# Optimization experiments

Hardware: AMD Instinct MI355X
Metric: run time of the kernel (lower is better)

The kernel has to match this reference:

```python
import jax, jax.numpy as jnp
import numpy as np

B, C, H, W = 16, 64, 1024, 16  # requires C*W == H per the module's implicit view/matmul constraint
C8 = C // 8


def setup_inputs() -> dict:
    key = jax.random.key(0)
    ks = jax.random.split(key, 7)
    s_in = 1.0 / np.sqrt(C)
    return {
        "x": jax.random.normal(ks[0], (B, C, H, W), dtype=jnp.float32),
        "Wq": jax.random.normal(ks[1], (C8, C), dtype=jnp.float32) * s_in,
        "bq": jax.random.normal(ks[2], (C8,), dtype=jnp.float32) * 0.01,
        "Wk": jax.random.normal(ks[3], (C8, C), dtype=jnp.float32) * s_in,
        "bk": jax.random.normal(ks[4], (C8,), dtype=jnp.float32) * 0.01,
        "Wv": jax.random.normal(ks[5], (C, C), dtype=jnp.float32) * s_in,
        "bv": jax.random.normal(ks[6], (C,), dtype=jnp.float32) * 0.01,
    }


def conv1x1(x, w, b):
    # 1x1 conv == per-pixel channel mixing: [B,C,H,W] x [O,C] -> [B,O,H,W]
    return jnp.einsum("bchw,oc->bohw", x, w) + b[None, :, None, None]


def reference(x, Wq, bq, Wk, bk, Wv, bv):
    b, c, h, w = x.shape
    q = conv1x1(x, Wq, bq)  # [B, C/8, H, W]
    k = conv1x1(x, Wk, bk)  # [B, C/8, H, W]
    v = conv1x1(x, Wv, bv)  # [B, C, H, W]
    # Faithful to torch .view(B, -1, H): row-major reshape, NOT a transpose.
    qf = jnp.swapaxes(q.reshape(b, -1, h), 1, 2)  # [B, H, C8*W]
    kf = k.reshape(b, -1, h)                      # [B, C8*W, H]
    vf = v.reshape(b, -1, h)                      # [B, C*W, H] (C*W == H)
    scores = jax.nn.softmax(jnp.matmul(qf, kf), axis=-1)  # [B, H, H]
    attended = jnp.matmul(scores, vf)             # [B, H, H]
    attended = attended.reshape(v.shape)          # [B, C, H, W]
    return x + attended
```

## Files before the change

### kernel.cpp

```cpp
#include <hip/hip_runtime.h>
#include <stdint.h>

typedef uint32_t u32;
typedef __attribute__((ext_vector_type(4))) float f32x4;
typedef __attribute__((ext_vector_type(8))) short short8;

#define NBATCH 16
#define NPIX   16384
#define NPB    1048576

__device__ __forceinline__ ushort f2bf(float f) {
  u32 b = __builtin_bit_cast(u32, f);
  return (ushort)((b + 0x7FFFu + ((b >> 16) & 1u)) >> 16);
}
__device__ __forceinline__ float bf2f(ushort h) {
  return __builtin_bit_cast(float, (u32)h << 16);
}

__device__ __forceinline__ void gload16(const void* g, void* l) {
  __builtin_amdgcn_global_load_lds(
      (const __attribute__((address_space(1))) u32*)g,
      (__attribute__((address_space(3))) u32*)l,
      16, 0, 0);
}

__global__ void prep_w2(const float* __restrict__ Wq, const float* __restrict__ bq,
                        const float* __restrict__ Wk, const float* __restrict__ bk,
                        const float* __restrict__ Wv, const float* __restrict__ bv,
                        ushort* __restrict__ Wpk, float* __restrict__ bpk)
{
  int gid = blockIdx.x * 256 + threadIdx.x;
  if (gid < 12288) {
    int m = gid >> 7, kk = gid & 127;
    int ch = kk & 63;
    ushort outv = 0;
    if (m < 8) {
      float wv = Wq[m * 64 + ch];
      ushort h = f2bf(wv);
      outv = (kk < 64) ? h : f2bf(wv - bf2f(h));
    } else if (m < 16) {
      float wv = Wk[(m - 8) * 64 + ch];
      ushort h = f2bf(wv);
      outv = (kk < 64) ? h : f2bf(wv - bf2f(h));
    } else if (m < 80) {
      outv = (kk < 64) ? f2bf(Wv[(m - 16) * 64 + ch]) : (ushort)0;
    }
    Wpk[gid] = outv;
  } else if (gid < 12368) {
    int o = gid - 12288;
    bpk[o] = (o < 8) ? bq[o] : (o < 16 ? bk[o - 8] : bv[o - 16]);
  }
}

__global__ __launch_bounds__(256) void proj12(
    const float* __restrict__ x, const ushort* __restrict__ Wpk,
    const float* __restrict__ bpk,
    ushort* __restrict__ Qt2, ushort* __restrict__ Kt2,
    ushort* __restrict__ Vt)
{
  __shared__ __align__(16) char smem[65536];
  int t = threadIdx.x;
  int w = t >> 6, lane = t & 63;
  int l15 = lane & 15, l4 = lane >> 4;

  int g = blockIdx.x;
  int lin = (g & 7) * 128 + (g >> 3);
  int b = lin >> 6;
  int l0 = (lin & 63) << 4;

  const uint4* Wp4 = (const uint4*)Wpk;
  uint4 Afrag[12];
  #pragma unroll
  for (int kc = 0; kc < 4; ++kc)
    Afrag[kc] = Wp4[l15 * 16 + kc * 4 + l4];
  #pragma unroll
  for (int mt = 1; mt < 5; ++mt)
    #pragma unroll
    for (int kc = 0; kc < 2; ++kc)
      Afrag[2 + mt * 2 + kc] = Wp4[(mt * 16 + l15) * 16 + kc * 4 + l4];
  __builtin_amdgcn_sched_barrier(0);

  #pragma unroll
  for (int c = 0; c < 2; ++c) {
    const float* xb = x + (size_t)b * NPB + l0 + c * 8;
    float* xs = (float*)(smem + c * 32768);
    #pragma unroll
    for (int it = 0; it < 8; ++it) {
      int f0 = (it * 4 + w) * 64;
      int f = f0 + lane;
      int ch = f >> 5, r2 = f & 31, tc = r2 >> 1, half = r2 & 1;
      gload16(xb + (size_t)ch * NPIX + tc * 1024 + half * 4, xs + f0 * 4);
    }
  }
  asm volatile("s_waitcnt vmcnt(8)" ::: "memory");
  __builtin_amdgcn_sched_barrier(0);
  __builtin_amdgcn_s_barrier();

  auto do_chunk = [&](char* region, int lc) {
    float* xs = (float*)region;
    f32x4 acc[5][2];
    #pragma unroll
    for (int mt = 0; mt < 5; ++mt) {
      f32x4 bv4;
      #pragma unroll
      for (int r = 0; r < 4; ++r) bv4[r] = bpk[mt * 16 + l4 * 4 + r];
      acc[mt][0] = bv4; acc[mt][1] = bv4;
    }
    #pragma unroll
    for (int i = 0; i < 2; ++i) {
      int px = (w * 2 + i) * 16 + l15;
      u32 xr[16];
      #pragma unroll
      for (int kc = 0; kc < 2; ++kc)
        #pragma unroll
        for (int j = 0; j < 8; ++j)
          xr[kc * 8 + j] = ((const u32*)xs)[(kc * 32 + l4 * 8 + j) * 128 + px];
      uint4 bxh[2], bxl[2];
      #pragma unroll
      for (int kc = 0; kc < 2; ++kc)
        #pragma unroll
        for (int p = 0; p < 4; ++p) {
          u32 a = xr[kc * 8 + 2 * p], cc = xr[kc * 8 + 2 * p + 1];
          ((u32*)&bxh[kc])[p] = (a >> 16) | (cc & 0xFFFF0000u);
          float fa = __builtin_bit_cast(float, a) -
                     __builtin_bit_cast(float, a & 0xFFFF0000u);
          float fc = __builtin_bit_cast(float, cc) -
                     __builtin_bit_cast(float, cc & 0xFFFF0000u);
          u32 la = __builtin_bit_cast(u32, fa), lc2 = __builtin_bit_cast(u32, fc);
          ((u32*)&bxl[kc])[p] = (la >> 16) | (lc2 & 0xFFFF0000u);
        }
      short8 h0 = __builtin_bit_cast(short8, bxh[0]);
      short8 h1 = __builtin_bit_cast(short8, bxh[1]);
      short8 s0 = __builtin_bit_cast(short8, bxl[0]);
      short8 s1 = __builtin_bit_cast(short8, bxl[1]);
      acc[0][i] = __builtin_amdgcn_mfma_f32_16x16x32_bf16(
          __builtin_bit_cast(short8, Afrag[0]), h0, acc[0][i], 0, 0, 0);
      acc[0][i] = __builtin_amdgcn_mfma_f32_16x16x32_bf16(
          __builtin_bit_cast(short8, Afrag[1]), h1, acc[0][i], 0, 0, 0);
      acc[0][i] = __builtin_amdgcn_mfma_f32_16x16x32_bf16(
          __builtin_bit_cast(short8, Afrag[0]), s0, acc[0][i], 0, 0, 0);
      acc[0][i] = __builtin_amdgcn_mfma_f32_16x16x32_bf16(
          __builtin_bit_cast(short8, Afrag[1]), s1, acc[0][i], 0, 0, 0);
      acc[0][i] = __builtin_amdgcn_mfma_f32_16x16x32_bf16(
          __builtin_bit_cast(short8, Afrag[2]), h0, acc[0][i], 0, 0, 0);
      acc[0][i] = __builtin_amdgcn_mfma_f32_16x16x32_bf16(
          __builtin_bit_cast(short8, Afrag[3]), h1, acc[0][i], 0, 0, 0);
      #pragma unroll
      for (int mt = 1; mt < 5; ++mt) {
        acc[mt][i] = __builtin_amdgcn_mfma_f32_16x16x32_bf16(
            __builtin_bit_cast(short8, Afrag[2 + mt * 2]), h0, acc[mt][i], 0, 0, 0);
        acc[mt][i] = __builtin_amdgcn_mfma_f32_16x16x32_bf16(
            __builtin_bit_cast(short8, Afrag[3 + mt * 2]), h1, acc[mt][i], 0, 0, 0);
      }
    }
    __syncthreads();

    float*  qkl = (float*)region;
    ushort* vl  = (ushort*)(region + 16 * 132 * 4);
    #pragma unroll
    for (int i = 0; i < 2; ++i) {
      int px = (w * 2 + i) * 16 + l15;
      #pragma unroll
      for (int r = 0; r < 4; ++r)
        qkl[(l4 * 4 + r) * 132 + px] = acc[0][i][r];
      #pragma unroll
      for (int mt = 1; mt < 5; ++mt)
        #pragma unroll
        for (int r = 0; r < 4; ++r)
          vl[((mt - 1) * 16 + l4 * 4 + r) * 136 + px] = f2bf(acc[mt][i][r]);
    }
    __syncthreads();

    if (t < 128) {
      int l = t >> 4, tcc = t & 15;
      size_t lrow = (size_t)b * 1024 + lc + l;
      int px = tcc * 8 + l;

      union { ushort s[8]; uint4 v; } qh, ql, kh, kl;
      #pragma unroll
      for (int o = 0; o < 8; ++o) {
        float qv = qkl[o * 132 + px];
        ushort h = f2bf(qv);
        qh.s[o] = h; ql.s[o] = f2bf(qv - bf2f(h));
        float kv = qkl[(8 + o) * 132 + px];
        h = f2bf(kv);
        kh.s[o] = h; kl.s[o] = f2bf(kv - bf2f(h));
      }
      ushort* qrow = Qt2 + lrow * 256 + tcc * 8;
      *(uint4*)qrow         = qh.v;
      *(uint4*)(qrow + 128) = ql.v;
      ushort* krow = Kt2 + lrow * 256 + tcc * 8;
      *(uint4*)krow         = kh.v;
      *(uint4*)(krow + 128) = kl.v;
    } else {
      int t2 = t - 128;
      int l = t2 >> 4, tcc = t2 & 15;
      size_t lrow = (size_t)b * 1024 + lc + l;

      ushort* vrow = Vt + lrow * 1024;
      #pragma unroll
      for (int it = 0; it < 4; ++it) {
        int c2 = (it << 4) + tcc;
        union { ushort s[16]; uint4 q[2]; } ov;
        #pragma unroll
        for (int tt = 0; tt < 16; ++tt)
          ov.s[tt] = vl[c2 * 136 + tt * 8 + l];
        *(uint4*)(vrow + c2 * 16)     = ov.q[0];
        *(uint4*)(vrow + c2 * 16 + 8) = ov.q[1];
      }
    }
  };

  do_chunk(smem, l0);
  do_chunk(smem + 32768, l0 + 8);
}

__global__ __launch_bounds__(512, 4) void gemm_qk2(
    const ushort* __restrict__ A,
    const ushort* __restrict__ B,
    float* __restrict__ C)
{
  __shared__ ushort Asm[8192];
  __shared__ ushort Bsm[16384];
  int t = threadIdx.x;

  int g = blockIdx.x;
  int lin = (g & 7) * 64 + (g >> 3);
  int bz = lin >> 5;
  int r5 = lin & 31;
  int by = r5 >> 2;
  int bx = r5 & 3;
  int m0 = by << 7, n0 = bx << 8;

  const ushort* Ab = A + (size_t)bz * 1024 * 256;
  const ushort* Bb = B + (size_t)bz * 1024 * 256;
  int w = t >> 6, lane = t & 63;
  int wm = w >> 2, wn = w & 3;
  int l15 = lane & 15, l4 = lane >> 4;

  int swc = (t & 7) ^ ((t >> 3) & 7);
  const ushort* pa = Ab + (size_t)(m0 + (t >> 3)) * 256 + swc * 8;
  const ushort* pb = Bb + (size_t)(n0 + (t >> 3)) * 256 + swc * 8;
  int wb = w * 512;

  constexpr int KA[6] = {0, 64, 128, 192, 0, 64};
  constexpr int KB[6] = {0, 64, 0, 64, 128, 192};

  f32x4 acc[4][4] = {};

  for (int it = 0; it < 6; ++it) {
    #pragma unroll
    for (int i = 0; i < 2; ++i)
      gload16(pa + (size_t)i * 64 * 256 + KA[it], Asm + i * 4096 + wb);
    #pragma unroll
    for (int i = 0; i < 4; ++i)
      gload16(pb + (size_t)i * 64 * 256 + KB[it], Bsm + i * 4096 + wb);
    __syncthreads();

    #pragma unroll
    for (int kk = 0; kk < 2; ++kk) {
      short8 af[4], bfr[4];
      #pragma unroll
      for (int mi = 0; mi < 4; ++mi) {
        int rr = (wm << 6) + (mi << 4) + l15;
        af[mi] = __builtin_bit_cast(short8,
            ((const uint4*)Asm)[rr * 8 + ((kk * 4 + l4) ^ (rr & 7))]);
      }
      #pragma unroll
      for (int ni = 0; ni < 4; ++ni) {
        int rr = (wn << 6) + (ni << 4) + l15;
        bfr[ni] = __builtin_bit_cast(short8,
            ((const uint4*)Bsm)[rr * 8 + ((kk * 4 + l4) ^ (rr & 7))]);
      }
      #pragma unroll
      for (int mi = 0; mi < 4; ++mi)
        #pragma unroll
        for (int ni = 0; ni < 4; ++ni)
          acc[mi][ni] = __builtin_amdgcn_mfma_f32_16x16x32_bf16(
              af[mi], bfr[ni], acc[mi][ni], 0, 0, 0);
    }
    __syncthreads();
  }

  #pragma unroll
  for (int mi = 0; mi < 4; ++mi) {
    int rbase = m0 + (wm << 6) + (mi << 4) + (l4 << 2);
    #pragma unroll
    for (int ni = 0; ni < 4; ++ni) {
      int col = n0 + (wn << 6) + (ni << 4) + l15;
      f32x4 v = acc[mi][ni];
      #pragma unroll
      for (int rr = 0; rr < 4; ++rr) {
        size_t idx = ((size_t)bz * 1024 + rbase + rr) * 1024 + col;
        C[idx] = v[rr];
      }
    }
  }
}

__global__ __launch_bounds__(512, 4) void gemm_pv(
    const ushort* __restrict__ A, int lda,
    const ushort* __restrict__ B, int ldb,
    float* __restrict__ C, const float* __restrict__ X)
{
  __shared__ ushort Asm[8192];
  __shared__ ushort Bsm[16384];
  int t = threadIdx.x;

  int g = blockIdx.x;
  int lin = (g & 7) * 64 + (g >> 3);
  int bz = lin >> 5;
  int r5 = lin & 31;
  int by = r5 >> 2;
  int bx = r5 & 3;
  int m0 = by << 7, n0 = bx << 8;

  const ushort* Ab = A + (size_t)bz * 1024 * lda;
  const ushort* Bb = B + (size_t)bz * 1024 * ldb;
  int w = t >> 6, lane = t & 63;
  int wm = w >> 2, wn = w & 3;
  int l15 = lane & 15, l4 = lane >> 4;

  int swc = (t & 7) ^ ((t >> 3) & 7);
  const ushort* pa = Ab + (size_t)(m0 + (t >> 3)) * lda + swc * 8;
  const ushort* pb = Bb + (size_t)(n0 + (t >> 3)) * ldb + swc * 8;
  int wb = w * 512;

  f32x4 acc[4][4] = {};

  for (int it = 0; it < 16; ++it) {
    int k0 = it * 64;
    #pragma unroll
    for (int i = 0; i < 2; ++i)
      gload16(pa + (size_t)i * 64 * lda + k0, Asm + i * 4096 + wb);
    #pragma unroll
    for (int i = 0; i < 4; ++i)
      gload16(pb + (size_t)i * 64 * ldb + k0, Bsm + i * 4096 + wb);
    __syncthreads();

    #pragma unroll
    for (int kk = 0; kk < 2; ++kk) {
      short8 af[4], bfr[4];
      #pragma unroll
      for (int mi = 0; mi < 4; ++mi) {
        int rr = (wm << 6) + (mi << 4) + l15;
        af[mi] = __builtin_bit_cast(short8,
            ((const uint4*)Asm)[rr * 8 + ((kk * 4 + l4) ^ (rr & 7))]);
      }
      #pragma unroll
      for (int ni = 0; ni < 4; ++ni) {
        int rr = (wn << 6) + (ni << 4) + l15;
        bfr[ni] = __builtin_bit_cast(short8,
            ((const uint4*)Bsm)[rr * 8 + ((kk * 4 + l4) ^ (rr & 7))]);
      }
      #pragma unroll
      for (int mi = 0; mi < 4; ++mi)
        #pragma unroll
        for (int ni = 0; ni < 4; ++ni)
          acc[mi][ni] = __builtin_amdgcn_mfma_f32_16x16x32_bf16(
              af[mi], bfr[ni], acc[mi][ni], 0, 0, 0);
    }
    __syncthreads();
  }

  #pragma unroll
  for (int mi = 0; mi < 4; ++mi) {
    int rbase = m0 + (wm << 6) + (mi << 4) + (l4 << 2);
    #pragma unroll
    for (int ni = 0; ni < 4; ++ni) {
      int col = n0 + (wn << 6) + (ni << 4) + l15;
      f32x4 v = acc[mi][ni];
      #pragma unroll
      for (int rr = 0; rr < 4; ++rr) {
        size_t idx = ((size_t)bz * 1024 + rbase + rr) * 1024 + col;
        C[idx] = v[rr] + X[idx];
      }
    }
  }
}

__global__ __launch_bounds__(256) void softmax_rows(float* __restrict__ S)
{
  size_t rowi = blockIdx.x;
  float* srow = S + rowi * 1024;
  int t = threadIdx.x;
  float4 v = ((const float4*)srow)[t];
  float m = fmaxf(fmaxf(v.x, v.y), fmaxf(v.z, v.w));
  #pragma unroll
  for (int off = 32; off > 0; off >>= 1) m = fmaxf(m, __shfl_xor(m, off));
  __shared__ float red[8];
  int wid = t >> 6, lane = t & 63;
  if (lane == 0) red[wid] = m;
  __syncthreads();
  m = fmaxf(fmaxf(red[0], red[1]), fmaxf(red[2], red[3]));
  float e0 = __expf(v.x - m), e1 = __expf(v.y - m);
  float e2 = __expf(v.z - m), e3 = __expf(v.w - m);
  float s = e0 + e1 + e2 + e3;
  #pragma unroll
  for (int off = 32; off > 0; off >>= 1) s += __shfl_xor(s, off);
  if (lane == 0) red[4 + wid] = s;
  __syncthreads();
  s = red[4] + red[5] + red[6] + red[7];
  float inv = 1.0f / s;
  union { ushort h[4]; uint2 q; } pk;
  pk.h[0] = f2bf(e0 * inv); pk.h[1] = f2bf(e1 * inv);
  pk.h[2] = f2bf(e2 * inv); pk.h[3] = f2bf(e3 * inv);
  ((uint2*)srow)[t] = pk.q;
}

extern "C" void kernel_launch(void* const* d_in, const int* in_sizes, int n_in,
                              void* d_out, int out_size, void* d_ws, size_t ws_size,
                              hipStream_t stream) {
  const float* x  = (const float*)d_in[0];
  const float* Wq = (const float*)d_in[1];
  const float* bq = (const float*)d_in[2];
  const float* Wk = (const float*)d_in[3];
  const float* bk = (const float*)d_in[4];
  const float* Wv = (const float*)d_in[5];
  const float* bv = (const float*)d_in[6];
  float* out = (float*)d_out;

  char* wsb = (char*)d_ws;
  ushort* Qt2 = (ushort*)wsb;
  ushort* Kt2 = (ushort*)(wsb + 8388608);
  ushort* Vt  = (ushort*)(wsb + 16777216);
  float*  S   = (float*)(wsb + 50331648);
  ushort* Wpk = (ushort*)(wsb + 117440512);
  float*  bpk = (float*)(wsb + 117440512 + 24576);

  prep_w2<<<49, 256, 0, stream>>>(Wq, bq, Wk, bk, Wv, bv, Wpk, bpk);
  proj12<<<1024, 256, 0, stream>>>(x, Wpk, bpk, Qt2, Kt2, Vt);
  gemm_qk2<<<512, 512, 0, stream>>>(Qt2, Kt2, S);
  softmax_rows<<<16384, 256, 0, stream>>>(S);
  gemm_pv<<<512, 512, 0, stream>>>((const ushort*)S, 2048, Vt, 1024, out, x);
}
```

Baseline: 125.1 us.

## Shrink GEMM tiles to 128x128 with 256 threads and widen projection to 512 threads

The QK and PV GEMMs move from 128x256 tiles with 512 threads (8 waves) to 128x128 tiles with 256 threads (4 waves). This doubles the grid to 1024 blocks, halves the B shared-memory buffer, and raises the occupancy hint to 5 blocks per CU. The projection kernel goes to 512 threads, so each wave handles one pixel group instead of two and issues half as many global-to-LDS loads. The aim is more parallelism and better load balance across CUs, at the cost of less data reuse per tile and extra redundant A/B loads. The wait count and loop trip counts are adjusted to match.

New measurement: 230.4 us. 1.84x slower.

```diff
diff --git a/kernel.cpp b/kernel.cpp
--- a/kernel.cpp
+++ b/kernel.cpp
@@ -52,7 +52,7 @@
   }
 }
 
-__global__ __launch_bounds__(256) void proj12(
+__global__ __launch_bounds__(512) void proj13(
     const float* __restrict__ x, const ushort* __restrict__ Wpk,
     const float* __restrict__ bpk,
     ushort* __restrict__ Qt2, ushort* __restrict__ Kt2,
@@ -85,30 +85,29 @@
     const float* xb = x + (size_t)b * NPB + l0 + c * 8;
     float* xs = (float*)(smem + c * 32768);
     #pragma unroll
-    for (int it = 0; it < 8; ++it) {
-      int f0 = (it * 4 + w) * 64;
+    for (int it = 0; it < 4; ++it) {
+      int f0 = (it * 8 + w) * 64;
       int f = f0 + lane;
       int ch = f >> 5, r2 = f & 31, tc = r2 >> 1, half = r2 & 1;
       gload16(xb + (size_t)ch * NPIX + tc * 1024 + half * 4, xs + f0 * 4);
     }
   }
-  asm volatile("s_waitcnt vmcnt(8)" ::: "memory");
+  asm volatile("s_waitcnt vmcnt(4)" ::: "memory");
   __builtin_amdgcn_sched_barrier(0);
   __builtin_amdgcn_s_barrier();
 
   auto do_chunk = [&](char* region, int lc) {
     float* xs = (float*)region;
-    f32x4 acc[5][2];
+    f32x4 acc[5];
     #pragma unroll
     for (int mt = 0; mt < 5; ++mt) {
       f32x4 bv4;
       #pragma unroll
       for (int r = 0; r < 4; ++r) bv4[r] = bpk[mt * 16 + l4 * 4 + r];
-      acc[mt][0] = bv4; acc[mt][1] = bv4;
-    }
-    #pragma unroll
-    for (int i = 0; i < 2; ++i) {
-      int px = (w * 2 + i) * 16 + l15;
+      acc[mt] = bv4;
+    }
+    {
+      int px = w * 16 + l15;
       u32 xr[16];
       #pragma unroll
       for (int kc = 0; kc < 2; ++kc)
@@ -133,41 +132,40 @@
       short8 h1 = __builtin_bit_cast(short8, bxh[1]);
       short8 s0 = __builtin_bit_cast(short8, bxl[0]);
       short8 s1 = __builtin_bit_cast(short8, bxl[1]);
-      acc[0][i] = __builtin_amdgcn_mfma_f32_16x16x32_bf16(
-          __builtin_bit_cast(short8, Afrag[0]), h0, acc[0][i], 0, 0, 0);
-      acc[0][i] = __builtin_amdgcn_mfma_f32_16x16x32_bf16(
-          __builtin_bit_cast(short8, Afrag[1]), h1, acc[0][i], 0, 0, 0);
-      acc[0][i] = __builtin_amdgcn_mfma_f32_16x16x32_bf16(
-          __builtin_bit_cast(short8, Afrag[0]), s0, acc[0][i], 0, 0, 0);
-      acc[0][i] = __builtin_amdgcn_mfma_f32_16x16x32_bf16(
-          __builtin_bit_cast(short8, Afrag[1]), s1, acc[0][i], 0, 0, 0);
-      acc[0][i] = __builtin_amdgcn_mfma_f32_16x16x32_bf16(
-          __builtin_bit_cast(short8, Afrag[2]), h0, acc[0][i], 0, 0, 0);
-      acc[0][i] = __builtin_amdgcn_mfma_f32_16x16x32_bf16(
-          __builtin_bit_cast(short8, Afrag[3]), h1, acc[0][i], 0, 0, 0);
+      acc[0] = __builtin_amdgcn_mfma_f32_16x16x32_bf16(
+          __builtin_bit_cast(short8, Afrag[0]), h0, acc[0], 0, 0, 0);
+      acc[0] = __builtin_amdgcn_mfma_f32_16x16x32_bf16(
+          __builtin_bit_cast(short8, Afrag[1]), h1, acc[0], 0, 0, 0);
+      acc[0] = __builtin_amdgcn_mfma_f32_16x16x32_bf16(
+          __builtin_bit_cast(short8, Afrag[0]), s0, acc[0], 0, 0, 0);
+      acc[0] = __builtin_amdgcn_mfma_f32_16x16x32_bf16(
+          __builtin_bit_cast(short8, Afrag[1]), s1, acc[0], 0, 0, 0);
+      acc[0] = __builtin_amdgcn_mfma_f32_16x16x32_bf16(
+          __builtin_bit_cast(short8, Afrag[2]), h0, acc[0], 0, 0, 0);
+      acc[0] = __builtin_amdgcn_mfma_f32_16x16x32_bf16(
+          __builtin_bit_cast(short8, Afrag[3]), h1, acc[0], 0, 0, 0);
       #pragma unroll
       for (int mt = 1; mt < 5; ++mt) {
-        acc[mt][i] = __builtin_amdgcn_mfma_f32_16x16x32_bf16(
-            __builtin_bit_cast(short8, Afrag[2 + mt * 2]), h0, acc[mt][i], 0, 0, 0);
-        acc[mt][i] = __builtin_amdgcn_mfma_f32_16x16x32_bf16(
-            __builtin_bit_cast(short8, Afrag[3 + mt * 2]), h1, acc[mt][i], 0, 0, 0);
+        acc[mt] = __builtin_amdgcn_mfma_f32_16x16x32_bf16(
+            __builtin_bit_cast(short8, Afrag[2 + mt * 2]), h0, acc[mt], 0, 0, 0);
+        acc[mt] = __builtin_amdgcn_mfma_f32_16x16x32_bf16(
+            __builtin_bit_cast(short8, Afrag[3 + mt * 2]), h1, acc[mt], 0, 0, 0);
       }
     }
     __syncthreads();
 
     float*  qkl = (float*)region;
     ushort* vl  = (ushort*)(region + 16 * 132 * 4);
-    #pragma unroll
-    for (int i = 0; i < 2; ++i) {
-      int px = (w * 2 + i) * 16 + l15;
+    {
+      int px = w * 16 + l15;
       #pragma unroll
       for (int r = 0; r < 4; ++r)
-        qkl[(l4 * 4 + r) * 132 + px] = acc[0][i][r];
+        qkl[(l4 * 4 + r) * 132 + px] = acc[0][r];
       #pragma unroll
       for (int mt = 1; mt < 5; ++mt)
         #pragma unroll
         for (int r = 0; r < 4; ++r)
-          vl[((mt - 1) * 16 + l4 * 4 + r) * 136 + px] = f2bf(acc[mt][i][r]);
+          vl[((mt - 1) * 16 + l4 * 4 + r) * 136 + px] = f2bf(acc[mt][r]);
     }
     __syncthreads();
 
@@ -192,7 +190,7 @@
       ushort* krow = Kt2 + lrow * 256 + tcc * 8;
       *(uint4*)krow         = kh.v;
       *(uint4*)(krow + 128) = kl.v;
-    } else {
+    } else if (t < 256) {
       int t2 = t - 128;
       int l = t2 >> 4, tcc = t2 & 15;
       size_t lrow = (size_t)b * 1024 + lc + l;
@@ -215,27 +213,26 @@
   do_chunk(smem + 32768, l0 + 8);
 }
 
-__global__ __launch_bounds__(512, 4) void gemm_qk2(
+__global__ __launch_bounds__(256, 5) void gemm_qk2(
     const ushort* __restrict__ A,
     const ushort* __restrict__ B,
     float* __restrict__ C)
 {
   __shared__ ushort Asm[8192];
-  __shared__ ushort Bsm[16384];
+  __shared__ ushort Bsm[8192];
   int t = threadIdx.x;
 
   int g = blockIdx.x;
-  int lin = (g & 7) * 64 + (g >> 3);
-  int bz = lin >> 5;
-  int r5 = lin & 31;
-  int by = r5 >> 2;
-  int bx = r5 & 3;
-  int m0 = by << 7, n0 = bx << 8;
+  int lin = (g & 7) * 128 + (g >> 3);
+  int bz = lin >> 6;
+  int by = (lin >> 3) & 7;
+  int bx = lin & 7;
+  int m0 = by << 7, n0 = bx << 7;
 
   const ushort* Ab = A + (size_t)bz * 1024 * 256;
   const ushort* Bb = B + (size_t)bz * 1024 * 256;
   int w = t >> 6, lane = t & 63;
-  int wm = w >> 2, wn = w & 3;
+  int wm = w >> 1, wn = w & 1;
   int l15 = lane & 15, l4 = lane >> 4;
 
   int swc = (t & 7) ^ ((t >> 3) & 7);
@@ -250,11 +247,11 @@
 
   for (int it = 0; it < 6; ++it) {
     #pragma unroll
-    for (int i = 0; i < 2; ++i)
-      gload16(pa + (size_t)i * 64 * 256 + KA[it], Asm + i * 4096 + wb);
-    #pragma unroll
     for (int i = 0; i < 4; ++i)
-      gload16(pb + (size_t)i * 64 * 256 + KB[it], Bsm + i * 4096 + wb);
+      gload16(pa + (size_t)i * 32 * 256 + KA[it], Asm + i * 2048 + wb);
+    #pragma unroll
+    for (int i = 0; i < 4; ++i)
+      gload16(pb + (size_t)i * 32 * 256 + KB[it], Bsm + i * 2048 + wb);
     __syncthreads();
 
     #pragma unroll
@@ -298,27 +295,26 @@
   }
 }
 
-__global__ __launch_bounds__(512, 4) void gemm_pv(
+__global__ __launch_bounds__(256, 5) void gemm_pv(
     const ushort* __restrict__ A, int lda,
     const ushort* __restrict__ B, int ldb,
     float* __restrict__ C, const float* __restrict__ X)
 {
   __shared__ ushort Asm[8192];
-  __shared__ ushort Bsm[16384];
+  __shared__ ushort Bsm[8192];
   int t = threadIdx.x;
 
   int g = blockIdx.x;
-  int lin = (g & 7) * 64 + (g >> 3);
-  int bz = lin >> 5;
-  int r5 = lin & 31;
-  int by = r5 >> 2;
-  int bx = r5 & 3;
-  int m0 = by << 7, n0 = bx << 8;
+  int lin = (g & 7) * 128 + (g >> 3);
+  int bz = lin >> 6;
+  int by = (lin >> 3) & 7;
+  int bx = lin & 7;
+  int m0 = by << 7, n0 = bx << 7;
 
   const ushort* Ab = A + (size_t)bz * 1024 * lda;
   const ushort* Bb = B + (size_t)bz * 1024 * ldb;
   int w = t >> 6, lane = t & 63;
-  int wm = w >> 2, wn = w & 3;
+  int wm = w >> 1, wn = w & 1;
   int l15 = lane & 15, l4 = lane >> 4;
 
   int swc = (t & 7) ^ ((t >> 3) & 7);
@@ -331,11 +327,11 @@
   for (int it = 0; it < 16; ++it) {
     int k0 = it * 64;
     #pragma unroll
-    for (int i = 0; i < 2; ++i)
-      gload16(pa + (size_t)i * 64 * lda + k0, Asm + i * 4096 + wb);
-    #pragma unroll
     for (int i = 0; i < 4; ++i)
-      gload16(pb + (size_t)i * 64 * ldb + k0, Bsm + i * 4096 + wb);
+      gload16(pa + (size_t)i * 32 * lda + k0, Asm + i * 2048 + wb);
+    #pragma unroll
+    for (int i = 0; i < 4; ++i)
+      gload16(pb + (size_t)i * 32 * ldb + k0, Bsm + i * 2048 + wb);
     __syncthreads();
 
     #pragma unroll
@@ -429,8 +425,8 @@
   float*  bpk = (float*)(wsb + 117440512 + 24576);
 
   prep_w2<<<49, 256, 0, stream>>>(Wq, bq, Wk, bk, Wv, bv, Wpk, bpk);
-  proj12<<<1024, 256, 0, stream>>>(x, Wpk, bpk, Qt2, Kt2, Vt);
-  gemm_qk2<<<512, 512, 0, stream>>>(Qt2, Kt2, S);
+  proj13<<<1024, 512, 0, stream>>>(x, Wpk, bpk, Qt2, Kt2, Vt);
+  gemm_qk2<<<1024, 256, 0, stream>>>(Qt2, Kt2, S);
   softmax_rows<<<16384, 256, 0, stream>>>(S);
-  gemm_pv<<<512, 512, 0, stream>>>((const ushort*)S, 2048, Vt, 1024, out, x);
-}
+  gemm_pv<<<1024, 256, 0, stream>>>((const ushort*)S, 2048, Vt, 1024, out, x);
+}
```
